# Kernel optimization log

Measured on AMD Instinct MI355X. Metric: run time of the kernel, lower is better.

## Reference

```python
import jax, jax.numpy as jnp
import numpy as np
import math

B, T, D, H = 2, 2048, 768, 12
ND = D // H  # head dim = 64


def precompute_freqs_cis(dim, end, theta=10000.0):
    freqs = 1.0 / (theta ** (jnp.arange(0, dim, 2, dtype=jnp.float32) / dim))  # [dim/2]
    t = jnp.arange(end, dtype=jnp.float32)
    freqs = jnp.outer(t, freqs)  # [end, dim/2]
    return jnp.cos(freqs), jnp.sin(freqs)


def apply_rotary_emb(q, k, cos, sin):
    # q, k: [b, t, h, nd]; cos/sin: [t, nd/2]
    def rot(x):
        xr, xi = x[..., 0::2], x[..., 1::2]  # even/odd interleaved split
        c = cos[None, :, None, :]
        s = sin[None, :, None, :]
        out_r = xr * c - xi * s
        out_i = xr * s + xi * c
        return jnp.stack([out_r, out_i], axis=-1).reshape(x.shape)
    return rot(q), rot(k)


def setup_inputs() -> dict:
    key = jax.random.key(0)
    ks = jax.random.split(key, 12)
    sc = 0.02
    q = jax.random.normal(ks[0], (B, T, D), dtype=jnp.float32)
    k = jax.random.normal(ks[1], (B, T, D), dtype=jnp.float32)
    v = jax.random.normal(ks[2], (B, T, D), dtype=jnp.float32)
    mask = jnp.tril(jnp.ones((T, T), dtype=jnp.int32))[None, None]  # causal [1,1,T,T]
    # weights stored as [d_in, d_out] (pre-transposed vs torch Linear)
    wq = jax.random.normal(ks[3], (D, D), dtype=jnp.float32) * sc
    bq = jax.random.normal(ks[4], (D,), dtype=jnp.float32) * sc
    wk = jax.random.normal(ks[5], (D, D), dtype=jnp.float32) * sc
    bk = jax.random.normal(ks[6], (D,), dtype=jnp.float32) * sc
    wv = jax.random.normal(ks[7], (D, D), dtype=jnp.float32) * sc
    bv = jax.random.normal(ks[8], (D,), dtype=jnp.float32) * sc
    wo = jax.random.normal(ks[9], (D, D), dtype=jnp.float32) * sc
    cos, sin = precompute_freqs_cis(ND, T)
    return {"q": q, "k": k, "v": v, "mask": mask, "wq": wq, "bq": bq,
            "wk": wk, "bk": bk, "wv": wv, "bv": bv, "wo": wo,
            "freqs_cos": cos, "freqs_sin": sin}


def reference(q, k, v, mask, wq, bq, wk, bk, wv, bv, wo, freqs_cos, freqs_sin):
    b, t, d = q.shape
    qh = (q @ wq + bq).reshape(b, t, H, ND)
    kh = (k @ wk + bk).reshape(b, t, H, ND)
    vh = (v @ wv + bv).reshape(b, t, H, ND).transpose(0, 2, 1, 3)  # [b,h,t,nd]
    qh, kh = apply_rotary_emb(qh, kh, freqs_cos[:t], freqs_sin[:t])
    qh = qh.transpose(0, 2, 1, 3)  # [b,h,t,nd]
    kh = kh.transpose(0, 2, 1, 3)
    attn = jnp.einsum('bhqd,bhkd->bhqk', qh, kh) / math.sqrt(ND)
    attn = jnp.where(mask == 0, jnp.float32(-jnp.inf), attn)
    probs = jax.nn.softmax(attn, axis=-1)
    out = jnp.einsum('bhqk,bhkd->bhqd', probs, vh)
    out = out.transpose(0, 2, 1, 3).reshape(b, t, d)
    return out @ wo
```

## Files before the change

### kernel.cpp

```cpp
#include <hip/hip_runtime.h>
#include <hip/hip_bf16.h>
#include <math.h>

#define BB 2
#define TT 2048
#define DD 768
#define HH 12
#define ND 64
#define MM (BB*TT)

typedef __attribute__((ext_vector_type(8))) short bf16x8;
typedef __attribute__((ext_vector_type(4))) float f32x4;
typedef __attribute__((ext_vector_type(16))) float f32x16;

__device__ __forceinline__ float bf2f(ushort u) {
    union { unsigned int i; float f; } v; v.i = ((unsigned int)u) << 16; return v.f;
}
__device__ __forceinline__ ushort f2bf(float f) {
    union { float f; unsigned int i; } v; v.f = f;
    unsigned int r = v.i + 0x7FFF + ((v.i >> 16) & 1);
    return (ushort)(r >> 16);
}

__device__ __forceinline__ void cp16(void* lds, const void* g) {
    __builtin_amdgcn_global_load_lds(
        (const __attribute__((address_space(1))) void*)g,
        (__attribute__((address_space(3))) void*)lds, 16, 0, 0);
}

__device__ __forceinline__ float fexp2(float x) {
    float r; asm("v_exp_f32 %0, %1" : "=v"(r) : "v"(x)); return r;
}
__device__ __forceinline__ unsigned int pk_bf16(float a, float b) {
    unsigned int r; asm("v_cvt_pk_bf16_f32 %0, %1, %2" : "=v"(r) : "v"(a), "v"(b)); return r;
}

__device__ __forceinline__ void plswap(unsigned int& a, unsigned int& b) {
#if __has_builtin(__builtin_amdgcn_permlane32_swap)
    auto r = __builtin_amdgcn_permlane32_swap(a, b, false, false);
    a = r[0]; b = r[1];
#else
    unsigned int sa = __shfl_xor((int)a, 32), sb = __shfl_xor((int)b, 32);
    bool hi = (threadIdx.x & 63) >= 32;
    unsigned int na = hi ? sb : a, nb = hi ? b : sa;
    a = na; b = nb;
#endif
}
__device__ __forceinline__ float partner32(float x, int hi) {
#if __has_builtin(__builtin_amdgcn_permlane32_swap)
    unsigned int u = __float_as_uint(x);
    auto r = __builtin_amdgcn_permlane32_swap(u, u, false, false);
    return __uint_as_float(hi ? r[0] : r[1]);
#else
    return __shfl_xor(x, 32);
#endif
}

#define QSCALE 0.18033688011112043f

__global__ __launch_bounds__(256) void conv_all(
    const float* __restrict__ x0, const float* __restrict__ x1, const float* __restrict__ x2,
    ushort* __restrict__ o0, ushort* __restrict__ o1, ushort* __restrict__ o2,
    const float* __restrict__ w0, const float* __restrict__ w1,
    const float* __restrict__ w2, const float* __restrict__ w3,
    ushort* __restrict__ t0, ushort* __restrict__ t1,
    ushort* __restrict__ t2, ushort* __restrict__ t3)
{
    const int z = blockIdx.z;
    if (blockIdx.x < 2048) {
        const float* x = z == 0 ? x0 : (z == 1 ? x1 : x2);
        ushort* o = z == 0 ? o0 : (z == 1 ? o1 : o2);
        const int total4 = MM * DD / 4;
        for (int i = blockIdx.x * 256 + threadIdx.x; i < total4; i += 2048 * 256) {
            float4 v = *(const float4*)&x[i * 4];
            ushort4 r;
            r.x = f2bf(v.x); r.y = f2bf(v.y); r.z = f2bf(v.z); r.w = f2bf(v.w);
            *(ushort4*)&o[i * 4] = r;
        }
    } else {
        __shared__ ushort tile[64][72];
        const int widx = z * 192 + (blockIdx.x - 2048);
        const int zz = widx / 144;
        const int tl = widx % 144;
        const float* w = zz == 0 ? w0 : zz == 1 ? w1 : zz == 2 ? w2 : w3;
        ushort* o = zz == 0 ? t0 : zz == 1 ? t1 : zz == 2 ? t2 : t3;
        const int n0 = (tl % (DD / 64)) * 64;
        const int k0 = (tl / (DD / 64)) * 64;
        #pragma unroll
        for (int it = 0; it < 4; ++it) {
            int e = (threadIdx.x + it * 256) * 4;
            int r = e >> 6, c = e & 63;
            float4 v = *(const float4*)&w[(size_t)(k0 + r) * DD + n0 + c];
            tile[c + 0][r] = f2bf(v.x);
            tile[c + 1][r] = f2bf(v.y);
            tile[c + 2][r] = f2bf(v.z);
            tile[c + 3][r] = f2bf(v.w);
        }
        __syncthreads();
        #pragma unroll
        for (int it = 0; it < 4; ++it) {
            int e = (threadIdx.x + it * 256) * 4;
            int nr = e >> 6, kc = e & 63;
            ushort4 r4;
            r4.x = tile[nr][kc + 0];
            r4.y = tile[nr][kc + 1];
            r4.z = tile[nr][kc + 2];
            r4.w = tile[nr][kc + 3];
            *(ushort4*)&o[(size_t)(n0 + nr) * DD + k0 + kc] = r4;
        }
    }
}

struct GArgs { const ushort* x; const ushort* wt; const float* bias; void* out;
               const float* cT; const float* sT; int rope; };

template<int MODE, int TM, int TN>
__global__ __launch_bounds__(256) void gemm_bf16(GArgs a0, GArgs a1, GArgs a2,
                                                 int nx, int ny)
{
    constexpr int WM = TM / 2, WN = TN / 2;
    constexpr int MF = WM / 16, NF = WN / 16;
    constexpr int ABYTES = TM * 128;
    constexpr int BUFB = (TM + TN) * 128;
    constexpr int NPASS = BUFB / 4096;
    constexpr int NK = DD / 64;
    __shared__ __align__(16) ushort S[2][BUFB / 2];
    const int tid = threadIdx.x;
    const int w = tid >> 6, l = tid & 63;
    const int wr = w >> 1, wc = w & 1;

    const int per = gridDim.x >> 3;
    const int p = blockIdx.x;
    const int task = (p & 7) * per + (p >> 3);
    const int bx = task % nx;
    const int by = (task / nx) % ny;
    const int bz = task / (nx * ny);
    GArgs ga = (bz == 0) ? a0 : (bz == 1 ? a1 : a2);
    const int n0 = bx * TN, m0 = by * TM;

    f32x4 acc[MF][NF] = {};

    auto stage = [&](int buf, int k0) {
        #pragma unroll
        for (int it = 0; it < NPASS; ++it) {
            const int ob = it * 4096 + w * 1024;
            const int o = ob + l * 16;
            if (ob < ABYTES) {
                const int row = o >> 7, inner = o & 127;
                cp16((char*)&S[buf][0] + ob,
                     (const char*)ga.x + (size_t)(m0 + row) * (DD * 2) + k0 * 2 +
                     (inner ^ ((row & 7) << 4)));
            } else {
                const int o2 = o - ABYTES;
                const int row = o2 >> 7, inner = o2 & 127;
                cp16((char*)&S[buf][0] + ob,
                     (const char*)ga.wt + (size_t)(n0 + row) * (DD * 2) + k0 * 2 +
                     (inner ^ ((row & 7) << 4)));
            }
        }
    };

    stage(0, 0);
    __syncthreads();
    const int lq = l >> 4, lr = l & 15;
    for (int t = 0; t < NK; ++t) {
        const int cur = t & 1;
        if (t + 1 < NK) stage(cur ^ 1, (t + 1) * 64);
        const char* ab = (const char*)&S[cur][0];
        #pragma unroll
        for (int kc = 0; kc < 2; ++kc) {
            const int kb = kc * 64 + lq * 16;
            bf16x8 af[MF], bfr[NF];
            #pragma unroll
            for (int i = 0; i < MF; ++i) {
                const int row = WM * wr + 16 * i + lr;
                af[i] = *(const bf16x8*)(ab + row * 128 + (kb ^ ((row & 7) << 4)));
            }
            #pragma unroll
            for (int j = 0; j < NF; ++j) {
                const int row = WN * wc + 16 * j + lr;
                bfr[j] = *(const bf16x8*)(ab + ABYTES + row * 128 + (kb ^ ((row & 7) << 4)));
            }
            __builtin_amdgcn_s_setprio(1);
            #pragma unroll
            for (int i = 0; i < MF; ++i)
                #pragma unroll
                for (int j = 0; j < NF; ++j)
                    acc[i][j] = __builtin_amdgcn_mfma_f32_16x16x32_bf16(af[i], bfr[j], acc[i][j], 0, 0, 0);
            __builtin_amdgcn_s_setprio(0);
        }
        __syncthreads();
    }

    if (MODE == 0 && ga.rope == -1) {
        ushort* tl = (ushort*)&S[0][0];
        #pragma unroll
        for (int i = 0; i < MF; ++i) {
            #pragma unroll
            for (int j = 0; j < NF; ++j) {
                #pragma unroll
                for (int r = 0; r < 4; ++r) {
                    const int ml = WM * wr + 16 * i + (l >> 4) * 4 + r;
                    const int nl = WN * wc + 16 * j + (l & 15);
                    tl[nl * (TM + 8) + ml] = f2bf(acc[i][j][r] + ga.bias[n0 + nl]);
                }
            }
        }
        __syncthreads();
        const int b = m0 >> 11, t0b = m0 & 2047;
        ushort* base = (ushort*)ga.out + ((size_t)(b * DD + n0)) * TT + t0b;
        #pragma unroll
        for (int it = 0; it < TM * TN / (256 * 8); ++it) {
            const int slot = tid + it * 256;
            const int d = slot / (TM / 8), c = (slot % (TM / 8)) * 8;
            bf16x8 v = *(const bf16x8*)&tl[d * (TM + 8) + c];
            *(bf16x8*)&base[(size_t)d * TT + c] = v;
        }
        return;
    }

    #pragma unroll
    for (int i = 0; i < MF; ++i) {
        #pragma unroll
        for (int j = 0; j < NF; ++j) {
            #pragma unroll
            for (int r = 0; r < 4; ++r) {
                const int m = m0 + WM * wr + 16 * i + (l >> 4) * 4 + r;
                const int n = n0 + WN * wc + 16 * j + (l & 15);
                float v = acc[i][j][r];
                if (MODE == 0) {
                    v += ga.bias[n];
                    const int tt = m & 2047;
                    if (ga.rope > 0) {
                        const int d = n & 63;
                        const float c = ga.cT[tt * 32 + (d >> 1)];
                        const float s = ga.sT[tt * 32 + (d >> 1)];
                        const float pv = __shfl_xor(v, 1);
                        v = (n & 1) ? (pv * s + v * c) : (v * c - pv * s);
                        if (ga.rope == 2) v *= QSCALE;
                    }
                    const int b = m >> 11;
                    const int h = n >> 6, d = n & 63;
                    ((ushort*)ga.out)[((size_t)(b * HH + h) * TT + tt) * ND + d] = f2bf(v);
                } else {
                    ((float*)ga.out)[(size_t)m * DD + n] = v;
                }
            }
        }
    }
}

#define NQB (TT/128)
#define NBH (BB*HH)
#define NTASK (NQB*NBH)
#define NCU 256

__global__ __launch_bounds__(512) void attn_mfma4(const ushort* __restrict__ Qh,
                                                  const ushort* __restrict__ Kh,
                                                  const ushort* __restrict__ VhT,
                                                  ushort* __restrict__ Op)
{
    __shared__ __align__(16) ushort Ks[2][2][4096];
    __shared__ __align__(16) ushort Vs[2][2][4096];
    const int tid = threadIdx.x;
    const int w = tid >> 6, l = tid & 63;
    const int lq = l & 31, hi = l >> 5;
    const int qs = w & 3;
    const int kvh = w >> 2;

    const int n = blockIdx.x;
    const int r_ = (n < NCU) ? n : (NTASK - 1 + NCU - n);
    const int qblk = (NQB - 1) - r_ / NBH;
    const int bh = r_ % NBH;

    const int q0 = qblk * 128;
    const int q0w = q0 + qs * 32;
    const int qg = q0w + lq;
    const int ntH = qblk + 1;
    const int kvbase = kvh * ntH * 64;

    const ushort* Qg = Qh + ((size_t)bh * TT + q0w) * ND;
    const ushort* Kg = Kh + (size_t)bh * TT * ND;
    const ushort* Vg = VhT + (size_t)bh * ND * TT;

    bf16x8 qf[4];
    #pragma unroll
    for (int ks = 0; ks < 4; ++ks)
        qf[ks] = *(const bf16x8*)((const char*)Qg + lq * 128 + ks * 32 + hi * 16);

    auto stageKV = [&](int buf, int kv0) {
        #pragma unroll
        for (int it = 0; it < 2; ++it) {
            int o = it * 4096 + qs * 1024 + l * 16;
            int row = o >> 7, inner = o & 127;
            int swz = inner ^ ((row & 7) << 4);
            cp16((char*)&Ks[kvh][buf][0] + it * 4096 + qs * 1024,
                 (const char*)Kg + (size_t)(kv0 + row) * 128 + swz);
            cp16((char*)&Vs[kvh][buf][0] + it * 4096 + qs * 1024,
                 (const char*)Vg + (size_t)row * (TT * 2) + kv0 * 2 + swz);
        }
    };

    float m = -1e30f, lsum = 0.f;
    f32x16 o0 = {}, o1 = {};

    stageKV(0, kvbase);
    __syncthreads();
    for (int t = 0; t < ntH; ++t) {
        const int cur = t & 1;
        if (t + 1 < ntH) stageKV(cur ^ 1, kvbase + (t + 1) * 64);
        const char* kb = (const char*)&Ks[kvh][cur][0];
        const char* vb = (const char*)&Vs[kvh][cur][0];
        const int kvt = kvbase + t * 64;

        if (kvt <= q0w + 31) {
            const bool have1 = (kvt + 32 <= q0w + 31);

            f32x16 st0 = {}, st1 = {};
            __builtin_amdgcn_s_setprio(1);
            #pragma unroll
            for (int ks = 0; ks < 4; ++ks) {
                bf16x8 kf = *(const bf16x8*)(kb + lq * 128 +
                                             ((ks * 32 + hi * 16) ^ ((lq & 7) << 4)));
                st0 = __builtin_amdgcn_mfma_f32_32x32x16_bf16(kf, qf[ks], st0, 0, 0, 0);
            }
            if (have1) {
                #pragma unroll
                for (int ks = 0; ks < 4; ++ks) {
                    bf16x8 kf = *(const bf16x8*)(kb + (32 + lq) * 128 +
                                                 ((ks * 32 + hi * 16) ^ ((lq & 7) << 4)));
                    st1 = __builtin_amdgcn_mfma_f32_32x32x16_bf16(kf, qf[ks], st1, 0, 0, 0);
                }
            }
            __builtin_amdgcn_s_setprio(0);

            float tm = -1e30f;
            if (kvt + 31 > q0w) {
                #pragma unroll
                for (int r = 0; r < 16; ++r) {
                    const int kvg = kvt + (r & 3) + 8 * (r >> 2) + 4 * hi;
                    float x = (kvg <= qg) ? st0[r] : -1e30f;
                    st0[r] = x;
                    tm = fmaxf(tm, x);
                }
            } else {
                #pragma unroll
                for (int r = 0; r < 16; ++r) tm = fmaxf(tm, st0[r]);
            }
            if (have1) {
                if (kvt + 63 > q0w) {
                    #pragma unroll
                    for (int r = 0; r < 16; ++r) {
                        const int kvg = kvt + 32 + (r & 3) + 8 * (r >> 2) + 4 * hi;
                        float x = (kvg <= qg) ? st1[r] : -1e30f;
                        st1[r] = x;
                        tm = fmaxf(tm, x);
                    }
                } else {
                    #pragma unroll
                    for (int r = 0; r < 16; ++r) tm = fmaxf(tm, st1[r]);
                }
            }
            tm = fmaxf(tm, partner32(tm, hi));

            const bool defer = __all(tm <= m + 11.5f);
            float alpha = 1.f;
            if (!defer) {
                const float nm = fmaxf(m, tm);
                alpha = fexp2(m - nm);
                m = nm;
            }

            float ps[16];
            unsigned int pkA[8], pkB[8];
            #pragma unroll
            for (int i = 0; i < 8; ++i) {
                const float p0 = fexp2(st0[2 * i + 0] - m);
                const float p1 = fexp2(st0[2 * i + 1] - m);
                pkA[i] = pk_bf16(p0, p1);
                ps[i] = p0 + p1;
            }
            if (have1) {
                #pragma unroll
                for (int i = 0; i < 8; ++i) {
                    const float p0 = fexp2(st1[2 * i + 0] - m);
                    const float p1 = fexp2(st1[2 * i + 1] - m);
                    pkB[i] = pk_bf16(p0, p1);
                    ps[8 + i] = p0 + p1;
                }
            } else {
                #pragma unroll
                for (int i = 0; i < 8; ++i) { pkB[i] = 0; ps[8 + i] = 0.f; }
            }
            const float t0s = (ps[0] + ps[1]) + (ps[2] + ps[3]);
            const float t1s = (ps[4] + ps[5]) + (ps[6] + ps[7]);
            const float t2s = (ps[8] + ps[9]) + (ps[10] + ps[11]);
            const float t3s = (ps[12] + ps[13]) + (ps[14] + ps[15]);
            float rs = (t0s + t1s) + (t2s + t3s);
            rs += partner32(rs, hi);
            lsum = lsum * alpha + rs;

            plswap(pkA[0], pkA[2]); plswap(pkA[1], pkA[3]);
            plswap(pkA[4], pkA[6]); plswap(pkA[5], pkA[7]);
            if (have1) {
                plswap(pkB[0], pkB[2]); plswap(pkB[1], pkB[3]);
                plswap(pkB[4], pkB[6]); plswap(pkB[5], pkB[7]);
            }
            union { unsigned int u[4]; bf16x8 v; } pa0, pa1, pa2, pa3;
            pa0.u[0] = pkA[0]; pa0.u[1] = pkA[1]; pa0.u[2] = pkA[2]; pa0.u[3] = pkA[3];
            pa1.u[0] = pkA[4]; pa1.u[1] = pkA[5]; pa1.u[2] = pkA[6]; pa1.u[3] = pkA[7];
            pa2.u[0] = pkB[0]; pa2.u[1] = pkB[1]; pa2.u[2] = pkB[2]; pa2.u[3] = pkB[3];
            pa3.u[0] = pkB[4]; pa3.u[1] = pkB[5]; pa3.u[2] = pkB[6]; pa3.u[3] = pkB[7];

            if (!defer) {
                #pragma unroll
                for (int r = 0; r < 16; ++r) { o0[r] *= alpha; o1[r] *= alpha; }
            }

            __builtin_amdgcn_s_setprio(1);
            #pragma unroll
            for (int sl = 0; sl < 2; ++sl) {
                const bf16x8 pf = sl == 0 ? pa0.v : pa1.v;
                const int cb = sl * 32 + hi * 16;
                bf16x8 va = *(const bf16x8*)(vb + lq * 128 + (cb ^ ((lq & 7) << 4)));
                bf16x8 vc = *(const bf16x8*)(vb + (lq + 32) * 128 + (cb ^ ((lq & 7) << 4)));
                o0 = __builtin_amdgcn_mfma_f32_32x32x16_bf16(va, pf, o0, 0, 0, 0);
                o1 = __builtin_amdgcn_mfma_f32_32x32x16_bf16(vc, pf, o1, 0, 0, 0);
            }
            if (have1) {
                #pragma unroll
                for (int sl = 0; sl < 2; ++sl) {
                    const bf16x8 pf = sl == 0 ? pa2.v : pa3.v;
                    const int cb = 64 + sl * 32 + hi * 16;
                    bf16x8 va = *(const bf16x8*)(vb + lq * 128 + (cb ^ ((lq & 7) << 4)));
                    bf16x8 vc = *(const bf16x8*)(vb + (lq + 32) * 128 + (cb ^ ((lq & 7) << 4)));
                    o0 = __builtin_amdgcn_mfma_f32_32x32x16_bf16(va, pf, o0, 0, 0, 0);
                    o1 = __builtin_amdgcn_mfma_f32_32x32x16_bf16(vc, pf, o1, 0, 0, 0);
                }
            }
            __builtin_amdgcn_s_setprio(0);
        }
        __syncthreads();
    }

    float* xO  = (float*)&Ks[0][0][0];
    float* xML = (float*)&Vs[0][0][0];
    if (kvh == 1) {
        float* dst = xO + qs * 2048;
        #pragma unroll
        for (int r = 0; r < 16; ++r) {
            dst[r * 64 + l] = o0[r];
            dst[(r + 16) * 64 + l] = o1[r];
        }
        if (hi == 0) { xML[qs * 64 + lq] = m; xML[qs * 64 + 32 + lq] = lsum; }
    }
    __syncthreads();
    if (kvh == 0) {
        const float* src = xO + qs * 2048;
        const float m1 = xML[qs * 64 + lq];
        const float l1 = xML[qs * 64 + 32 + lq];
        const float ms = fmaxf(m, m1);
        const float a0 = fexp2(m - ms), a1 = fexp2(m1 - ms);
        const float inv = 1.0f / (lsum * a0 + l1 * a1);
        const int b = bh / HH, h = bh % HH;
        ushort* dst = Op + ((size_t)(b * TT + qg)) * DD + h * ND;
        #pragma unroll
        for (int g = 0; g < 4; ++g) {
            ushort4 w0, w1;
            w0.x = f2bf((o0[4 * g + 0] * a0 + src[(4 * g + 0) * 64 + l] * a1) * inv);
            w0.y = f2bf((o0[4 * g + 1] * a0 + src[(4 * g + 1) * 64 + l] * a1) * inv);
            w0.z = f2bf((o0[4 * g + 2] * a0 + src[(4 * g + 2) * 64 + l] * a1) * inv);
            w0.w = f2bf((o0[4 * g + 3] * a0 + src[(4 * g + 3) * 64 + l] * a1) * inv);
            *(ushort4*)&dst[8 * g + 4 * hi] = w0;
            w1.x = f2bf((o1[4 * g + 0] * a0 + src[(16 + 4 * g + 0) * 64 + l] * a1) * inv);
            w1.y = f2bf((o1[4 * g + 1] * a0 + src[(16 + 4 * g + 1) * 64 + l] * a1) * inv);
            w1.z = f2bf((o1[4 * g + 2] * a0 + src[(16 + 4 * g + 2) * 64 + l] * a1) * inv);
            w1.w = f2bf((o1[4 * g + 3] * a0 + src[(16 + 4 * g + 3) * 64 + l] * a1) * inv);
            *(ushort4*)&dst[32 + 8 * g + 4 * hi] = w1;
        }
    }
}

extern "C" void kernel_launch(void* const* d_in, const int* in_sizes, int n_in,
                              void* d_out, int out_size, void* d_ws, size_t ws_size,
                              hipStream_t stream)
{
    const float* q  = (const float*)d_in[0];
    const float* k  = (const float*)d_in[1];
    const float* v  = (const float*)d_in[2];
    const float* wq = (const float*)d_in[4];
    const float* bq = (const float*)d_in[5];
    const float* wk = (const float*)d_in[6];
    const float* bk = (const float*)d_in[7];
    const float* wv = (const float*)d_in[8];
    const float* bv = (const float*)d_in[9];
    const float* wo = (const float*)d_in[10];
    const float* fc = (const float*)d_in[11];
    const float* fs = (const float*)d_in[12];
    float* out = (float*)d_out;

    ushort* qB  = (ushort*)d_ws;
    ushort* kB  = qB  + (size_t)MM * DD;
    ushort* vB  = kB  + (size_t)MM * DD;
    ushort* wqT = vB  + (size_t)MM * DD;
    ushort* wkT = wqT + (size_t)DD * DD;
    ushort* wvT = wkT + (size_t)DD * DD;
    ushort* woT = wvT + (size_t)DD * DD;
    ushort* Qh  = woT + (size_t)DD * DD;
    ushort* Kh  = Qh  + (size_t)MM * DD;
    ushort* VhT = Kh  + (size_t)MM * DD;
    ushort* Op  = qB;

    conv_all<<<dim3(2240, 1, 3), 256, 0, stream>>>(q, k, v, qB, kB, vB,
                                                   wq, wk, wv, wo, wqT, wkT, wvT, woT);

    GArgs aq{qB, wqT, bq, (void*)Qh, fc, fs, 2};
    GArgs ak{kB, wkT, bk, (void*)Kh, fc, fs, 1};
    GArgs av{vB, wvT, bv, (void*)VhT, nullptr, nullptr, -1};
    gemm_bf16<0, 128, 64><<<dim3(1152), 256, 0, stream>>>(aq, ak, av, DD / 64, MM / 128);

    attn_mfma4<<<dim3(NTASK), 512, 0, stream>>>(Qh, Kh, VhT, Op);

    GArgs ao{Op, woT, nullptr, (void*)out, nullptr, nullptr, 0};
    gemm_bf16<1, 64, 64><<<dim3(768), 256, 0, stream>>>(ao, ao, ao, DD / 64, MM / 64);
}
```

Before: 95.56 us.

## Fuse fp32-to-bf16 activation conversion into QKV projection GEMM A-tile loads

Drops the separate pass that converted q, k and v from fp32 to bf16 in workspace. The QKV GEMM now loads fp32 A tiles straight into registers, packs them to bf16, and writes them swizzled into LDS after the MFMA compute, overlapped with async loads of the B tile. This removes a full write and re-read of the converted activations. In exchange the GEMM reads twice as many A bytes, holds more registers, and A loads are now synchronous register loads rather than async copies. It relies on pk_bf16, which sits in the part of the file not shown.

```diff
diff --git a/kernel.cpp b/kernel.cpp
--- a/kernel.cpp
+++ b/kernel.cpp
@@ -58,60 +58,44 @@
 
 #define QSCALE 0.18033688011112043f
 
-__global__ __launch_bounds__(256) void conv_all(
-    const float* __restrict__ x0, const float* __restrict__ x1, const float* __restrict__ x2,
-    ushort* __restrict__ o0, ushort* __restrict__ o1, ushort* __restrict__ o2,
+__global__ __launch_bounds__(256) void conv_w(
     const float* __restrict__ w0, const float* __restrict__ w1,
     const float* __restrict__ w2, const float* __restrict__ w3,
     ushort* __restrict__ t0, ushort* __restrict__ t1,
     ushort* __restrict__ t2, ushort* __restrict__ t3)
 {
-    const int z = blockIdx.z;
-    if (blockIdx.x < 2048) {
-        const float* x = z == 0 ? x0 : (z == 1 ? x1 : x2);
-        ushort* o = z == 0 ? o0 : (z == 1 ? o1 : o2);
-        const int total4 = MM * DD / 4;
-        for (int i = blockIdx.x * 256 + threadIdx.x; i < total4; i += 2048 * 256) {
-            float4 v = *(const float4*)&x[i * 4];
-            ushort4 r;
-            r.x = f2bf(v.x); r.y = f2bf(v.y); r.z = f2bf(v.z); r.w = f2bf(v.w);
-            *(ushort4*)&o[i * 4] = r;
-        }
-    } else {
-        __shared__ ushort tile[64][72];
-        const int widx = z * 192 + (blockIdx.x - 2048);
-        const int zz = widx / 144;
-        const int tl = widx % 144;
-        const float* w = zz == 0 ? w0 : zz == 1 ? w1 : zz == 2 ? w2 : w3;
-        ushort* o = zz == 0 ? t0 : zz == 1 ? t1 : zz == 2 ? t2 : t3;
-        const int n0 = (tl % (DD / 64)) * 64;
-        const int k0 = (tl / (DD / 64)) * 64;
-        #pragma unroll
-        for (int it = 0; it < 4; ++it) {
-            int e = (threadIdx.x + it * 256) * 4;
-            int r = e >> 6, c = e & 63;
-            float4 v = *(const float4*)&w[(size_t)(k0 + r) * DD + n0 + c];
-            tile[c + 0][r] = f2bf(v.x);
-            tile[c + 1][r] = f2bf(v.y);
-            tile[c + 2][r] = f2bf(v.z);
-            tile[c + 3][r] = f2bf(v.w);
-        }
-        __syncthreads();
-        #pragma unroll
-        for (int it = 0; it < 4; ++it) {
-            int e = (threadIdx.x + it * 256) * 4;
-            int nr = e >> 6, kc = e & 63;
-            ushort4 r4;
-            r4.x = tile[nr][kc + 0];
-            r4.y = tile[nr][kc + 1];
-            r4.z = tile[nr][kc + 2];
-            r4.w = tile[nr][kc + 3];
-            *(ushort4*)&o[(size_t)(n0 + nr) * DD + k0 + kc] = r4;
-        }
-    }
-}
-
-struct GArgs { const ushort* x; const ushort* wt; const float* bias; void* out;
+    __shared__ ushort tile[64][72];
+    const int zz = blockIdx.z;
+    const float* w = zz == 0 ? w0 : zz == 1 ? w1 : zz == 2 ? w2 : w3;
+    ushort* o = zz == 0 ? t0 : zz == 1 ? t1 : zz == 2 ? t2 : t3;
+    const int n0 = (blockIdx.x % (DD / 64)) * 64;
+    const int k0 = (blockIdx.x / (DD / 64)) * 64;
+    #pragma unroll
+    for (int it = 0; it < 4; ++it) {
+        int e = (threadIdx.x + it * 256) * 4;
+        int r = e >> 6, c = e & 63;
+        float4 v = *(const float4*)&w[(size_t)(k0 + r) * DD + n0 + c];
+        tile[c + 0][r] = f2bf(v.x);
+        tile[c + 1][r] = f2bf(v.y);
+        tile[c + 2][r] = f2bf(v.z);
+        tile[c + 3][r] = f2bf(v.w);
+    }
+    __syncthreads();
+    #pragma unroll
+    for (int it = 0; it < 4; ++it) {
+        int e = (threadIdx.x + it * 256) * 4;
+        int nr = e >> 6, kc = e & 63;
+        ushort4 r4;
+        r4.x = tile[nr][kc + 0];
+        r4.y = tile[nr][kc + 1];
+        r4.z = tile[nr][kc + 2];
+        r4.w = tile[nr][kc + 3];
+        *(ushort4*)&o[(size_t)(n0 + nr) * DD + k0 + kc] = r4;
+    }
+}
+
+struct GArgs { const float* xf; const ushort* x; const ushort* wt;
+               const float* bias; void* out;
                const float* cT; const float* sT; int rope; };
 
 template<int MODE, int TM, int TN>
@@ -123,6 +107,8 @@
     constexpr int ABYTES = TM * 128;
     constexpr int BUFB = (TM + TN) * 128;
     constexpr int NPASS = BUFB / 4096;
+    constexpr int APASS = TM * 128 / 4096;
+    constexpr int BPASS = TN * 128 / 4096;
     constexpr int NK = DD / 64;
     __shared__ __align__(16) ushort S[2][BUFB / 2];
     const int tid = threadIdx.x;
@@ -139,8 +125,42 @@
     const int n0 = bx * TN, m0 = by * TM;
 
     f32x4 acc[MF][NF] = {};
-
-    auto stage = [&](int buf, int k0) {
+    float4 ra[APASS][2];
+
+    auto loadA = [&](int k0) {
+        #pragma unroll
+        for (int it = 0; it < APASS; ++it) {
+            const int o = it * 4096 + w * 1024 + l * 16;
+            const int row = o >> 7, inner = o & 127;
+            const int swz = inner ^ ((row & 7) << 4);
+            const float* src = ga.xf + (size_t)(m0 + row) * DD + k0 + (swz >> 1);
+            ra[it][0] = *(const float4*)src;
+            ra[it][1] = *(const float4*)(src + 4);
+        }
+    };
+    auto writeA = [&](int buf) {
+        #pragma unroll
+        for (int it = 0; it < APASS; ++it) {
+            const int ob = it * 4096 + w * 1024;
+            union { unsigned int u[4]; bf16x8 v; } pk4;
+            pk4.u[0] = pk_bf16(ra[it][0].x, ra[it][0].y);
+            pk4.u[1] = pk_bf16(ra[it][0].z, ra[it][0].w);
+            pk4.u[2] = pk_bf16(ra[it][1].x, ra[it][1].y);
+            pk4.u[3] = pk_bf16(ra[it][1].z, ra[it][1].w);
+            *(bf16x8*)((char*)&S[buf][0] + ob + l * 16) = pk4.v;
+        }
+    };
+    auto stageB = [&](int buf, int k0) {
+        #pragma unroll
+        for (int it = 0; it < BPASS; ++it) {
+            const int o2 = it * 4096 + w * 1024 + l * 16;
+            const int row = o2 >> 7, inner = o2 & 127;
+            cp16((char*)&S[buf][0] + ABYTES + it * 4096 + w * 1024,
+                 (const char*)ga.wt + (size_t)(n0 + row) * (DD * 2) + k0 * 2 +
+                 (inner ^ ((row & 7) << 4)));
+        }
+    };
+    auto stageAll = [&](int buf, int k0) {
         #pragma unroll
         for (int it = 0; it < NPASS; ++it) {
             const int ob = it * 4096 + w * 1024;
@@ -160,12 +180,8 @@
         }
     };
 
-    stage(0, 0);
-    __syncthreads();
     const int lq = l >> 4, lr = l & 15;
-    for (int t = 0; t < NK; ++t) {
-        const int cur = t & 1;
-        if (t + 1 < NK) stage(cur ^ 1, (t + 1) * 64);
+    auto compute = [&](int cur) {
         const char* ab = (const char*)&S[cur][0];
         #pragma unroll
         for (int kc = 0; kc < 2; ++kc) {
@@ -189,7 +205,30 @@
                     acc[i][j] = __builtin_amdgcn_mfma_f32_16x16x32_bf16(af[i], bfr[j], acc[i][j], 0, 0, 0);
             __builtin_amdgcn_s_setprio(0);
         }
+    };
+
+    if constexpr (MODE == 0) {
+        loadA(0);
+        stageB(0, 0);
+        writeA(0);
         __syncthreads();
+        for (int t = 0; t < NK; ++t) {
+            const int cur = t & 1;
+            const bool more = (t + 1 < NK);
+            if (more) { loadA((t + 1) * 64); stageB(cur ^ 1, (t + 1) * 64); }
+            compute(cur);
+            if (more) writeA(cur ^ 1);
+            __syncthreads();
+        }
+    } else {
+        stageAll(0, 0);
+        __syncthreads();
+        for (int t = 0; t < NK; ++t) {
+            const int cur = t & 1;
+            if (t + 1 < NK) stageAll(cur ^ 1, (t + 1) * 64);
+            compute(cur);
+            __syncthreads();
+        }
     }
 
     if (MODE == 0 && ga.rope == -1) {
@@ -499,28 +538,24 @@
     const float* fs = (const float*)d_in[12];
     float* out = (float*)d_out;
 
-    ushort* qB  = (ushort*)d_ws;
-    ushort* kB  = qB  + (size_t)MM * DD;
-    ushort* vB  = kB  + (size_t)MM * DD;
-    ushort* wqT = vB  + (size_t)MM * DD;
+    ushort* wqT = (ushort*)d_ws;
     ushort* wkT = wqT + (size_t)DD * DD;
     ushort* wvT = wkT + (size_t)DD * DD;
     ushort* woT = wvT + (size_t)DD * DD;
     ushort* Qh  = woT + (size_t)DD * DD;
     ushort* Kh  = Qh  + (size_t)MM * DD;
     ushort* VhT = Kh  + (size_t)MM * DD;
-    ushort* Op  = qB;
-
-    conv_all<<<dim3(2240, 1, 3), 256, 0, stream>>>(q, k, v, qB, kB, vB,
-                                                   wq, wk, wv, wo, wqT, wkT, wvT, woT);
-
-    GArgs aq{qB, wqT, bq, (void*)Qh, fc, fs, 2};
-    GArgs ak{kB, wkT, bk, (void*)Kh, fc, fs, 1};
-    GArgs av{vB, wvT, bv, (void*)VhT, nullptr, nullptr, -1};
+    ushort* Op  = VhT + (size_t)MM * DD;
+
+    conv_w<<<dim3(144, 1, 4), 256, 0, stream>>>(wq, wk, wv, wo, wqT, wkT, wvT, woT);
+
+    GArgs aq{q, nullptr, wqT, bq, (void*)Qh, fc, fs, 2};
+    GArgs ak{k, nullptr, wkT, bk, (void*)Kh, fc, fs, 1};
+    GArgs av{v, nullptr, wvT, bv, (void*)VhT, nullptr, nullptr, -1};
     gemm_bf16<0, 128, 64><<<dim3(1152), 256, 0, stream>>>(aq, ak, av, DD / 64, MM / 128);
 
     attn_mfma4<<<dim3(NTASK), 512, 0, stream>>>(Qh, Kh, VhT, Op);
 
-    GArgs ao{Op, woT, nullptr, (void*)out, nullptr, nullptr, 0};
+    GArgs ao{nullptr, Op, woT, nullptr, (void*)out, nullptr, nullptr, 0};
     gemm_bf16<1, 64, 64><<<dim3(768), 256, 0, stream>>>(ao, ao, ao, DD / 64, MM / 64);
 }
```

New measurement: 97.11 us. No clear change (+1.6%).
